# Kernel optimization log

Measured on AMD Instinct MI355X. Metric: run time of the kernel, lower is better.

## Reference

```python
import jax, jax.numpy as jnp
import numpy as np

N = 50000      # nodes
E = 800000     # edges (avg degree 16)
D_IN, D_H, D_OUT = 128, 256, 128


def setup_inputs() -> dict:
    key = jax.random.key(0)
    ks = jax.random.split(key, 8)
    x = jax.random.normal(ks[0], (N, D_IN), dtype=jnp.float32)
    edge_index = jax.random.randint(ks[1], (2, E), 0, N, dtype=jnp.int64)
    s1 = 1.0 / np.sqrt(D_IN).astype(np.float32)
    s2 = 1.0 / np.sqrt(D_H).astype(np.float32)
    return {
        "x": x,
        "edge_index": edge_index,
        "W1l": jax.random.normal(ks[2], (D_H, D_IN), jnp.float32) * s1,
        "b1l": jnp.zeros((D_H,), jnp.float32),
        "W1r": jax.random.normal(ks[3], (D_H, D_IN), jnp.float32) * s1,
        "W2l": jax.random.normal(ks[4], (D_OUT, D_H), jnp.float32) * s2,
        "b2l": jnp.zeros((D_OUT,), jnp.float32),
        "W2r": jax.random.normal(ks[5], (D_OUT, D_H), jnp.float32) * s2,
    }


def sage_conv(x, src, dst, Wl, bl, Wr):
    # mean-aggregate source features into destination nodes
    agg = jax.ops.segment_sum(x[src], dst, num_segments=N)           # [N, d_in]
    deg = jax.ops.segment_sum(jnp.ones((src.shape[0],), x.dtype), dst, num_segments=N)
    mean = agg / jnp.maximum(deg, 1.0)[:, None]
    # lin_l(mean_agg) + lin_r(x_root); lin_r has no bias (PyG SAGEConv default)
    return mean @ Wl.T + bl + x @ Wr.T


def reference(x, edge_index, W1l, b1l, W1r, W2l, b2l, W2r):
    src, dst = edge_index[0], edge_index[1]
    h = sage_conv(x, src, dst, W1l, b1l, W1r)
    h = jax.nn.relu(h)  # dropout inactive in eval mode
    return sage_conv(h, src, dst, W2l, b2l, W2r)
```

## Files before the change

kernel.cpp:

```cpp
#include <hip/hip_runtime.h>


typedef __attribute__((ext_vector_type(8))) short bf16x8;
typedef __attribute__((ext_vector_type(4))) float floatx4;

__device__ inline unsigned short f2b(float f) {
  unsigned int x = __float_as_uint(f);
  unsigned int r = (x + 0x7fffu + ((x >> 16) & 1u)) >> 16;
  return (unsigned short)r;
}
__device__ inline float blo(unsigned int u) { return __uint_as_float(u << 16); }
__device__ inline float bhi(unsigned int u) { return __uint_as_float(u & 0xffff0000u); }

#define ACC8(A, u)                                            \
  {                                                           \
    A[0] += blo((u).x); A[1] += bhi((u).x);                   \
    A[2] += blo((u).y); A[3] += bhi((u).y);                   \
    A[4] += blo((u).z); A[5] += bhi((u).z);                   \
    A[6] += blo((u).w); A[7] += bhi((u).w);                   \
  }

__global__ void prep_kernel(const float* __restrict__ x,
                            const float* __restrict__ W1l, const float* __restrict__ W1r,
                            const float* __restrict__ W2l, const float* __restrict__ W2r,
                            unsigned short* __restrict__ Wc1, unsigned short* __restrict__ Wc2,
                            unsigned short* __restrict__ A1,
                            int* __restrict__ cnt, int* __restrict__ off, int N, int E) {
  int i = blockIdx.x * blockDim.x + threadIdx.x;
  if (i < 65536) {
    int j = i >> 8, k = i & 255;
    float v1 = (k < 128) ? W1l[j * 128 + k] : W1r[j * 128 + (k - 128)];
    Wc1[i] = f2b(v1);
    float v2 = (j < 128) ? W2l[j * 256 + k] : W2r[(j - 128) * 256 + k];
    Wc2[i] = f2b(v2);
  }
  if (i < N) cnt[i] = 0;
  if (i == 0) off[N] = E;
  if (i < N * 32) {
    int n = i >> 5, c = (i & 31) * 4;
    float4 v = *(const float4*)(x + (size_t)n * 128 + c);
    uint2 p;
    p.x = (unsigned int)f2b(v.x) | ((unsigned int)f2b(v.y) << 16);
    p.y = (unsigned int)f2b(v.z) | ((unsigned int)f2b(v.w) << 16);
    *(uint2*)(A1 + (size_t)n * 256 + 128 + c) = p;
  }
}

__global__ void hist_kernel(const int* __restrict__ dst, int* __restrict__ cnt,
                            int* __restrict__ rank, int E) {
  int i = blockIdx.x * blockDim.x + threadIdx.x;
  int e = i * 4;
  if (e + 3 < E) {
    int4 d = *(const int4*)(dst + e);
    int4 r;
    r.x = atomicAdd(&cnt[d.x], 1);
    r.y = atomicAdd(&cnt[d.y], 1);
    r.z = atomicAdd(&cnt[d.z], 1);
    r.w = atomicAdd(&cnt[d.w], 1);
    *(int4*)(rank + e) = r;
  } else {
    for (; e < E; e++) rank[e] = atomicAdd(&cnt[dst[e]], 1);
  }
}

__global__ __launch_bounds__(1024) void scan_blocks_kernel(const int* __restrict__ cnt,
                                                           int* __restrict__ off,
                                                           int* __restrict__ bsum, int N) {
  __shared__ int wsum[16];
  __shared__ int wincl[16];
  const int tid = threadIdx.x;
  const int lane = tid & 63;
  const int wv = tid >> 6;
  const int i = blockIdx.x * 1024 + tid;
  const int v = (i < N) ? cnt[i] : 0;
  int s = v;
#pragma unroll
  for (int o = 1; o < 64; o <<= 1) {
    int t = __shfl_up(s, o, 64);
    if (lane >= o) s += t;
  }
  if (lane == 63) wsum[wv] = s;
  __syncthreads();
  if (tid < 16) {
    int ws = wsum[tid];
#pragma unroll
    for (int o = 1; o < 16; o <<= 1) {
      int t = __shfl_up(ws, o, 16);
      if ((tid & 15) >= o) ws += t;
    }
    wincl[tid] = ws;
  }
  __syncthreads();
  const int wo = wv ? wincl[wv - 1] : 0;
  if (i < N) off[i] = wo + s - v;
  if (tid == 1023) bsum[blockIdx.x] = wo + s;
}

__global__ __launch_bounds__(1024) void scan_add_kernel(int* __restrict__ off,
                                                        const int* __restrict__ bsum, int N, int SB) {
  __shared__ int bofs[64];
  const int tid = threadIdx.x;
  if (tid < 64) {
    int v = (tid < SB) ? bsum[tid] : 0;
    int s = v;
#pragma unroll
    for (int o = 1; o < 64; o <<= 1) {
      int t = __shfl_up(s, o, 64);
      if (tid >= o) s += t;
    }
    bofs[tid] = s - v;
  }
  __syncthreads();
  int i = blockIdx.x * 1024 + tid;
  if (i < N) off[i] = off[i] + bofs[blockIdx.x];
}

__global__ void fill_kernel(const int* __restrict__ src, const int* __restrict__ dst,
                            const int* __restrict__ rank, const int* __restrict__ off,
                            int* __restrict__ csr, int E) {
  int i = blockIdx.x * blockDim.x + threadIdx.x;
  int e = i * 4;
  if (e + 3 < E) {
    int4 d = *(const int4*)(dst + e);
    int4 r = *(const int4*)(rank + e);
    int4 s = *(const int4*)(src + e);
    csr[off[d.x] + r.x] = s.x;
    csr[off[d.y] + r.y] = s.y;
    csr[off[d.z] + r.z] = s.z;
    csr[off[d.w] + r.w] = s.w;
  } else {
    for (; e < E; e++) csr[off[dst[e]] + rank[e]] = src[e];
  }
}

__global__ void gather1_kernel(const unsigned short* __restrict__ feat,
                               const int* __restrict__ csr, const int* __restrict__ off,
                               unsigned short* __restrict__ ob, int N) {
  int wid = (blockIdx.x * blockDim.x + threadIdx.x) >> 6;
  if (wid >= N) return;
  const int lane = threadIdx.x & 63;
  const int slot = lane >> 3;
  const int j = lane & 7;
  const int c0 = j * 8;
  const int s0 = off[wid], s1 = off[wid + 1];
  float a[16] = {};
  int e = s0 + slot;
  for (; e + 8 < s1; e += 16) {
    int i0 = csr[e], i1 = csr[e + 8];
    uint4 u0 = *(const uint4*)(feat + (size_t)i0 * 256 + c0);
    uint4 v0 = *(const uint4*)(feat + (size_t)i0 * 256 + 64 + c0);
    uint4 u1 = *(const uint4*)(feat + (size_t)i1 * 256 + c0);
    uint4 v1 = *(const uint4*)(feat + (size_t)i1 * 256 + 64 + c0);
    ACC8(a, u0); ACC8((a + 8), v0);
    ACC8(a, u1); ACC8((a + 8), v1);
  }
  for (; e < s1; e += 8) {
    int i0 = csr[e];
    uint4 u0 = *(const uint4*)(feat + (size_t)i0 * 256 + c0);
    uint4 v0 = *(const uint4*)(feat + (size_t)i0 * 256 + 64 + c0);
    ACC8(a, u0); ACC8((a + 8), v0);
  }
#pragma unroll
  for (int k = 0; k < 16; k++) {
    a[k] += __shfl_xor(a[k], 8, 64);
    a[k] += __shfl_xor(a[k], 16, 64);
    a[k] += __shfl_xor(a[k], 32, 64);
  }
  if (slot == 0) {
    const float inv = 1.0f / fmaxf((float)(s1 - s0), 1.0f);
    uint4 p;
    p.x = (unsigned int)f2b(a[0] * inv) | ((unsigned int)f2b(a[1] * inv) << 16);
    p.y = (unsigned int)f2b(a[2] * inv) | ((unsigned int)f2b(a[3] * inv) << 16);
    p.z = (unsigned int)f2b(a[4] * inv) | ((unsigned int)f2b(a[5] * inv) << 16);
    p.w = (unsigned int)f2b(a[6] * inv) | ((unsigned int)f2b(a[7] * inv) << 16);
    *(uint4*)(ob + (size_t)wid * 256 + c0) = p;
    p.x = (unsigned int)f2b(a[8] * inv) | ((unsigned int)f2b(a[9] * inv) << 16);
    p.y = (unsigned int)f2b(a[10] * inv) | ((unsigned int)f2b(a[11] * inv) << 16);
    p.z = (unsigned int)f2b(a[12] * inv) | ((unsigned int)f2b(a[13] * inv) << 16);
    p.w = (unsigned int)f2b(a[14] * inv) | ((unsigned int)f2b(a[15] * inv) << 16);
    *(uint4*)(ob + (size_t)wid * 256 + 64 + c0) = p;
  }
}

__global__ void gather2_kernel(const unsigned short* __restrict__ t,
                               const int* __restrict__ csr, const int* __restrict__ off,
                               float* __restrict__ out, int N) {
  int wid = (blockIdx.x * blockDim.x + threadIdx.x) >> 6;
  if (wid >= N) return;
  const int lane = threadIdx.x & 63;
  const int slot = lane >> 3;
  const int j = lane & 7;
  const int c0 = j * 8;
  const int s0 = off[wid], s1 = off[wid + 1];
  float a[16] = {};
  int e = s0 + slot;
  for (; e + 8 < s1; e += 16) {
    int i0 = csr[e], i1 = csr[e + 8];
    uint4 u0 = *(const uint4*)(t + (size_t)i0 * 128 + c0);
    uint4 v0 = *(const uint4*)(t + (size_t)i0 * 128 + 64 + c0);
    uint4 u1 = *(const uint4*)(t + (size_t)i1 * 128 + c0);
    uint4 v1 = *(const uint4*)(t + (size_t)i1 * 128 + 64 + c0);
    ACC8(a, u0); ACC8((a + 8), v0);
    ACC8(a, u1); ACC8((a + 8), v1);
  }
  for (; e < s1; e += 8) {
    int i0 = csr[e];
    uint4 u0 = *(const uint4*)(t + (size_t)i0 * 128 + c0);
    uint4 v0 = *(const uint4*)(t + (size_t)i0 * 128 + 64 + c0);
    ACC8(a, u0); ACC8((a + 8), v0);
  }
#pragma unroll
  for (int k = 0; k < 16; k++) {
    a[k] += __shfl_xor(a[k], 8, 64);
    a[k] += __shfl_xor(a[k], 16, 64);
    a[k] += __shfl_xor(a[k], 32, 64);
  }
  if (slot == 0) {
    const float inv = 1.0f / fmaxf((float)(s1 - s0), 1.0f);
    float4* o0 = (float4*)(out + (size_t)wid * 128 + c0);
    float4* o1 = (float4*)(out + (size_t)wid * 128 + 64 + c0);
    float4 r0 = o0[0], r1 = o0[1], r2 = o1[0], r3 = o1[1];
    r0.x += a[0] * inv;  r0.y += a[1] * inv;  r0.z += a[2] * inv;  r0.w += a[3] * inv;
    r1.x += a[4] * inv;  r1.y += a[5] * inv;  r1.z += a[6] * inv;  r1.w += a[7] * inv;
    r2.x += a[8] * inv;  r2.y += a[9] * inv;  r2.z += a[10] * inv; r2.w += a[11] * inv;
    r3.x += a[12] * inv; r3.y += a[13] * inv; r3.z += a[14] * inv; r3.w += a[15] * inv;
    o0[0] = r0; o0[1] = r1; o1[0] = r2; o1[1] = r3;
  }
}

template <int MODE>
__global__ __launch_bounds__(256, 2)
void gemm_bf16(const unsigned short* __restrict__ A, const unsigned short* __restrict__ W,
               const float* __restrict__ bias, unsigned short* __restrict__ Hout,
               float* __restrict__ Fout, int M) {
  constexpr int LDA = 72;
  __shared__ __align__(16) unsigned short As[128 * LDA];
  __shared__ __align__(16) unsigned short Ws[128 * LDA];
  const int t = threadIdx.x;
  const int lane = t & 63;
  const int wave = t >> 6;
  const int wm = (wave & 1) * 64;
  const int wn = (wave >> 1) * 64;
  const int l15 = lane & 15;
  const int quad = lane >> 4;
  const int m_blk = blockIdx.x * 128;
  const int j_blk = blockIdx.y * 128;

  floatx4 acc[4][4] = {};

  for (int kc = 0; kc < 256; kc += 64) {
    __syncthreads();
#pragma unroll
    for (int i = 0; i < 4; i++) {
      int c = t + 256 * i;
      int row = c >> 3;
      int col = (c & 7) * 8;
      int ar = m_blk + row;
      if (ar >= M) ar = M - 1;
      uint4 av = *(const uint4*)(A + (size_t)ar * 256 + kc + col);
      *(uint4*)(As + row * LDA + col) = av;
      uint4 wv = *(const uint4*)(W + (size_t)(j_blk + row) * 256 + kc + col);
      *(uint4*)(Ws + row * LDA + col) = wv;
    }
    __syncthreads();
#pragma unroll
    for (int ks = 0; ks < 64; ks += 32) {
      bf16x8 af[4], bfr[4];
#pragma unroll
      for (int mt = 0; mt < 4; mt++)
        af[mt] = *(const bf16x8*)(As + (wm + mt * 16 + l15) * LDA + ks + quad * 8);
#pragma unroll
      for (int nt = 0; nt < 4; nt++)
        bfr[nt] = *(const bf16x8*)(Ws + (wn + nt * 16 + l15) * LDA + ks + quad * 8);
#pragma unroll
      for (int mt = 0; mt < 4; mt++)
#pragma unroll
        for (int nt = 0; nt < 4; nt++)
          acc[mt][nt] = __builtin_amdgcn_mfma_f32_16x16x32_bf16(af[mt], bfr[nt], acc[mt][nt], 0, 0, 0);
    }
  }

#pragma unroll
  for (int mt = 0; mt < 4; mt++) {
#pragma unroll
    for (int nt = 0; nt < 4; nt++) {
      const int jl = wn + nt * 16 + l15;
      float bv = 0.f;
      if (MODE == 0) bv = bias[j_blk + jl];
      else if (j_blk != 0) bv = bias[jl];
#pragma unroll
      for (int r = 0; r < 4; r++) {
        const int node = m_blk + wm + mt * 16 + quad * 4 + r;
        if (node >= M) continue;
        const float v = acc[mt][nt][r];
        if (MODE == 0) {
          Hout[(size_t)node * 256 + j_blk + jl] = f2b(fmaxf(v + bv, 0.f));
        } else if (j_blk == 0) {
          Hout[(size_t)node * 128 + jl] = f2b(v);
        } else {
          Fout[(size_t)node * 128 + jl] = v + bv;
        }
      }
    }
  }
}

extern "C" void kernel_launch(void* const* d_in, const int* in_sizes, int n_in,
                              void* d_out, int out_size, void* d_ws, size_t ws_size,
                              hipStream_t stream) {
  const float* x   = (const float*)d_in[0];
  const int*  eidx = (const int*)d_in[1];
  const float* W1l = (const float*)d_in[2];
  const float* b1l = (const float*)d_in[3];
  const float* W1r = (const float*)d_in[4];
  const float* W2l = (const float*)d_in[5];
  const float* b2l = (const float*)d_in[6];
  const float* W2r = (const float*)d_in[7];
  float* out = (float*)d_out;

  const int N = in_sizes[0] / 128;
  const int E = in_sizes[1] / 2;
  const int* src = eidx;
  const int* dst = eidx + E;

  int* cnt  = (int*)d_ws;
  int* off  = cnt + N;
  int* bsum = off + N + 1;
  int* rank = bsum + 64;
  int* csr  = rank + E;
  size_t ioff = ((size_t)(N + N + 1 + 64 + 2 * E) * 4 + 15) & ~(size_t)15;
  unsigned short* A1  = (unsigned short*)((char*)d_ws + ioff);
  unsigned short* h   = A1 + (size_t)N * 256;
  unsigned short* tb  = h + (size_t)N * 256;
  unsigned short* Wc1 = tb + (size_t)N * 128;
  unsigned short* Wc2 = Wc1 + 65536;

  const int SB = (N + 1023) / 1024;

  prep_kernel<<<(N * 32 + 255) / 256, 256, 0, stream>>>(x, W1l, W1r, W2l, W2r,
                                                        Wc1, Wc2, A1, cnt, off, N, E);
  hist_kernel<<<(E / 4 + 255) / 256, 256, 0, stream>>>(dst, cnt, rank, E);
  scan_blocks_kernel<<<SB, 1024, 0, stream>>>(cnt, off, bsum, N);
  scan_add_kernel<<<SB, 1024, 0, stream>>>(off, bsum, N, SB);
  fill_kernel<<<(E / 4 + 255) / 256, 256, 0, stream>>>(src, dst, rank, off, csr, E);

  const int gblocks = (N + 3) / 4;
  gather1_kernel<<<gblocks, 256, 0, stream>>>(A1 + 128, csr, off, A1, N);

  dim3 gg((N + 127) / 128, 2);
  gemm_bf16<0><<<gg, 256, 0, stream>>>(A1, Wc1, b1l, h, nullptr, N);
  gemm_bf16<1><<<gg, 256, 0, stream>>>(h, Wc2, b2l, tb, out, N);
  gather2_kernel<<<gblocks, 256, 0, stream>>>(tb, csr, off, out, N);
}
```

Baseline: 274.1 us.

## Fuse CSR build and first gather into one cooperative persistent kernel

Merges prep, histogram, two-level scan, CSR fill and the layer-1 gather into a single cooperative kernel that uses grid-wide syncs between phases instead of six separate launches. The scan is rewritten for 256-thread blocks handling 4 elements per thread, with the block offset taken as a prefix of the block sums. This targets per-launch overhead and the tail bubbles between short dependent kernels. In exchange it adds grid.sync costs and host-side occupancy queries on every call, and the grid-stride persistent loops may be less efficient than the original wide launches. It falls back to the old launch sequence if the cooperative launch fails.

Result: slower. 812.9 us (+196.6%).

```diff
diff --git a/kernel.cpp b/kernel.cpp
--- a/kernel.cpp
+++ b/kernel.cpp
@@ -1,4 +1,7 @@
 #include <hip/hip_runtime.h>
+#include <hip/hip_cooperative_groups.h>
+
+namespace cg = cooperative_groups;
 
 
 typedef __attribute__((ext_vector_type(8))) short bf16x8;
@@ -20,47 +23,221 @@
     A[6] += blo((u).w); A[7] += bhi((u).w);                   \
   }
 
+
+__device__ inline void ph_prep(int tid, int nthreads,
+                               const float* __restrict__ x,
+                               const float* __restrict__ W1l, const float* __restrict__ W1r,
+                               const float* __restrict__ W2l, const float* __restrict__ W2r,
+                               unsigned short* __restrict__ Wc1, unsigned short* __restrict__ Wc2,
+                               unsigned short* __restrict__ A1,
+                               int* __restrict__ cnt, int* __restrict__ off, int N, int E) {
+  for (int i = tid; i < N * 32; i += nthreads) {
+    int n = i >> 5, c = (i & 31) * 4;
+    float4 v = *(const float4*)(x + (size_t)n * 128 + c);
+    uint2 p;
+    p.x = (unsigned int)f2b(v.x) | ((unsigned int)f2b(v.y) << 16);
+    p.y = (unsigned int)f2b(v.z) | ((unsigned int)f2b(v.w) << 16);
+    *(uint2*)(A1 + (size_t)n * 256 + 128 + c) = p;
+  }
+  for (int i = tid; i < 65536; i += nthreads) {
+    int j = i >> 8, k = i & 255;
+    float v1 = (k < 128) ? W1l[j * 128 + k] : W1r[j * 128 + (k - 128)];
+    Wc1[i] = f2b(v1);
+    float v2 = (j < 128) ? W2l[j * 256 + k] : W2r[(j - 128) * 256 + k];
+    Wc2[i] = f2b(v2);
+  }
+  for (int i = tid; i < N; i += nthreads) cnt[i] = 0;
+  if (tid == 0) off[N] = E;
+}
+
+__device__ inline void ph_hist(int tid, int nthreads, const int* __restrict__ dst,
+                               int* __restrict__ cnt, int* __restrict__ rank, int E) {
+  for (int e = tid * 4; e < E; e += nthreads * 4) {
+    if (e + 3 < E) {
+      int4 d = *(const int4*)(dst + e);
+      int4 r;
+      r.x = atomicAdd(&cnt[d.x], 1);
+      r.y = atomicAdd(&cnt[d.y], 1);
+      r.z = atomicAdd(&cnt[d.z], 1);
+      r.w = atomicAdd(&cnt[d.w], 1);
+      *(int4*)(rank + e) = r;
+    } else {
+      for (int q = e; q < E; q++) rank[q] = atomicAdd(&cnt[dst[q]], 1);
+    }
+  }
+}
+
+__device__ inline void ph_fill(int tid, int nthreads,
+                               const int* __restrict__ src, const int* __restrict__ dst,
+                               const int* __restrict__ rank, const int* __restrict__ off,
+                               int* __restrict__ csr, int E) {
+  for (int e = tid * 4; e < E; e += nthreads * 4) {
+    if (e + 3 < E) {
+      int4 d = *(const int4*)(dst + e);
+      int4 r = *(const int4*)(rank + e);
+      int4 s4 = *(const int4*)(src + e);
+      csr[off[d.x] + r.x] = s4.x;
+      csr[off[d.y] + r.y] = s4.y;
+      csr[off[d.z] + r.z] = s4.z;
+      csr[off[d.w] + r.w] = s4.w;
+    } else {
+      for (int q = e; q < E; q++) csr[off[dst[q]] + rank[q]] = src[q];
+    }
+  }
+}
+
+__device__ inline void ph_gather1_one(int wid, int lane,
+                                      const unsigned short* __restrict__ feat,
+                                      const int* __restrict__ csr, const int* __restrict__ off,
+                                      unsigned short* __restrict__ A1) {
+  const int slot = lane >> 3;
+  const int c0 = (lane & 7) * 8;
+  const int s0 = off[wid], s1 = off[wid + 1];
+  float a[16] = {};
+  int e = s0 + slot;
+  for (; e + 8 < s1; e += 16) {
+    int i0 = csr[e], i1 = csr[e + 8];
+    uint4 u0 = *(const uint4*)(feat + (size_t)i0 * 256 + c0);
+    uint4 v0 = *(const uint4*)(feat + (size_t)i0 * 256 + 64 + c0);
+    uint4 u1 = *(const uint4*)(feat + (size_t)i1 * 256 + c0);
+    uint4 v1 = *(const uint4*)(feat + (size_t)i1 * 256 + 64 + c0);
+    ACC8(a, u0); ACC8((a + 8), v0);
+    ACC8(a, u1); ACC8((a + 8), v1);
+  }
+  for (; e < s1; e += 8) {
+    int i0 = csr[e];
+    uint4 u0 = *(const uint4*)(feat + (size_t)i0 * 256 + c0);
+    uint4 v0 = *(const uint4*)(feat + (size_t)i0 * 256 + 64 + c0);
+    ACC8(a, u0); ACC8((a + 8), v0);
+  }
+#pragma unroll
+  for (int k = 0; k < 16; k++) {
+    a[k] += __shfl_xor(a[k], 8, 64);
+    a[k] += __shfl_xor(a[k], 16, 64);
+    a[k] += __shfl_xor(a[k], 32, 64);
+  }
+  if (slot == 0) {
+    const float inv = 1.0f / fmaxf((float)(s1 - s0), 1.0f);
+    uint4 p;
+    p.x = (unsigned int)f2b(a[0] * inv) | ((unsigned int)f2b(a[1] * inv) << 16);
+    p.y = (unsigned int)f2b(a[2] * inv) | ((unsigned int)f2b(a[3] * inv) << 16);
+    p.z = (unsigned int)f2b(a[4] * inv) | ((unsigned int)f2b(a[5] * inv) << 16);
+    p.w = (unsigned int)f2b(a[6] * inv) | ((unsigned int)f2b(a[7] * inv) << 16);
+    *(uint4*)(A1 + (size_t)wid * 256 + c0) = p;
+    p.x = (unsigned int)f2b(a[8] * inv) | ((unsigned int)f2b(a[9] * inv) << 16);
+    p.y = (unsigned int)f2b(a[10] * inv) | ((unsigned int)f2b(a[11] * inv) << 16);
+    p.z = (unsigned int)f2b(a[12] * inv) | ((unsigned int)f2b(a[13] * inv) << 16);
+    p.w = (unsigned int)f2b(a[14] * inv) | ((unsigned int)f2b(a[15] * inv) << 16);
+    *(uint4*)(A1 + (size_t)wid * 256 + 64 + c0) = p;
+  }
+}
+
+__global__ __launch_bounds__(256, 8)
+void build_gather_kernel(const float* __restrict__ x,
+                         const float* __restrict__ W1l, const float* __restrict__ W1r,
+                         const float* __restrict__ W2l, const float* __restrict__ W2r,
+                         unsigned short* __restrict__ Wc1, unsigned short* __restrict__ Wc2,
+                         unsigned short* __restrict__ A1,
+                         int* __restrict__ cnt, int* __restrict__ off,
+                         int* __restrict__ bsum, int* __restrict__ rank,
+                         int* __restrict__ csr,
+                         const int* __restrict__ src, const int* __restrict__ dst,
+                         int N, int E, int SB) {
+  cg::grid_group grid = cg::this_grid();
+  __shared__ int wsum[4];
+  __shared__ int bofsS;
+  const int tid = blockIdx.x * blockDim.x + threadIdx.x;
+  const int nthreads = gridDim.x * blockDim.x;
+
+  ph_prep(tid, nthreads, x, W1l, W1r, W2l, W2r, Wc1, Wc2, A1, cnt, off, N, E);
+  grid.sync();
+  ph_hist(tid, nthreads, dst, cnt, rank, E);
+  grid.sync();
+
+  const int b = blockIdx.x;
+  if (b < SB) {
+    const int base = b * 1024 + threadIdx.x * 4;
+    int4 v = make_int4(0, 0, 0, 0);
+    if (base + 3 < N) v = *(const int4*)(cnt + base);
+    else {
+      if (base < N) v.x = cnt[base];
+      if (base + 1 < N) v.y = cnt[base + 1];
+      if (base + 2 < N) v.z = cnt[base + 2];
+    }
+    const int tsum = v.x + v.y + v.z + v.w;
+    const int lane = threadIdx.x & 63;
+    const int wv = threadIdx.x >> 6;
+    int s = tsum;
+#pragma unroll
+    for (int o = 1; o < 64; o <<= 1) {
+      int t = __shfl_up(s, o, 64);
+      if (lane >= o) s += t;
+    }
+    if (lane == 63) wsum[wv] = s;
+    __syncthreads();
+    int wo = 0;
+#pragma unroll
+    for (int w = 0; w < 4; w++) wo += (w < wv) ? wsum[w] : 0;
+    const int excl = wo + s - tsum;
+    int4 o4;
+    o4.x = excl; o4.y = excl + v.x; o4.z = o4.y + v.y; o4.w = o4.z + v.z;
+    if (base + 3 < N) *(int4*)(off + base) = o4;
+    else {
+      if (base < N) off[base] = o4.x;
+      if (base + 1 < N) off[base + 1] = o4.y;
+      if (base + 2 < N) off[base + 2] = o4.z;
+    }
+    if (threadIdx.x == 255) bsum[b] = wo + s;
+  }
+  grid.sync();
+
+  if (b > 0 && b < SB) {
+    if (threadIdx.x < 64) {
+      int v = (threadIdx.x < b) ? bsum[threadIdx.x] : 0;
+#pragma unroll
+      for (int o = 1; o < 64; o <<= 1) v += __shfl_xor(v, o, 64);
+      if (threadIdx.x == 0) bofsS = v;
+    }
+    __syncthreads();
+    const int bofs = bofsS;
+    const int base = b * 1024 + threadIdx.x * 4;
+    if (base + 3 < N) {
+      int4 o4 = *(const int4*)(off + base);
+      o4.x += bofs; o4.y += bofs; o4.z += bofs; o4.w += bofs;
+      *(int4*)(off + base) = o4;
+    } else {
+      if (base < N) off[base] += bofs;
+      if (base + 1 < N) off[base + 1] += bofs;
+      if (base + 2 < N) off[base + 2] += bofs;
+    }
+  }
+  grid.sync();
+
+  ph_fill(tid, nthreads, src, dst, rank, off, csr, E);
+  grid.sync();
+
+  const int nwaves = nthreads >> 6;
+  const int lane = threadIdx.x & 63;
+  const unsigned short* feat = A1 + 128;
+  for (int wid = tid >> 6; wid < N; wid += nwaves)
+    ph_gather1_one(wid, lane, feat, csr, off, A1);
+}
+
+
 __global__ void prep_kernel(const float* __restrict__ x,
                             const float* __restrict__ W1l, const float* __restrict__ W1r,
                             const float* __restrict__ W2l, const float* __restrict__ W2r,
                             unsigned short* __restrict__ Wc1, unsigned short* __restrict__ Wc2,
                             unsigned short* __restrict__ A1,
                             int* __restrict__ cnt, int* __restrict__ off, int N, int E) {
-  int i = blockIdx.x * blockDim.x + threadIdx.x;
-  if (i < 65536) {
-    int j = i >> 8, k = i & 255;
-    float v1 = (k < 128) ? W1l[j * 128 + k] : W1r[j * 128 + (k - 128)];
-    Wc1[i] = f2b(v1);
-    float v2 = (j < 128) ? W2l[j * 256 + k] : W2r[(j - 128) * 256 + k];
-    Wc2[i] = f2b(v2);
-  }
-  if (i < N) cnt[i] = 0;
-  if (i == 0) off[N] = E;
-  if (i < N * 32) {
-    int n = i >> 5, c = (i & 31) * 4;
-    float4 v = *(const float4*)(x + (size_t)n * 128 + c);
-    uint2 p;
-    p.x = (unsigned int)f2b(v.x) | ((unsigned int)f2b(v.y) << 16);
-    p.y = (unsigned int)f2b(v.z) | ((unsigned int)f2b(v.w) << 16);
-    *(uint2*)(A1 + (size_t)n * 256 + 128 + c) = p;
-  }
+  int tid = blockIdx.x * blockDim.x + threadIdx.x;
+  ph_prep(tid, gridDim.x * blockDim.x, x, W1l, W1r, W2l, W2r, Wc1, Wc2, A1, cnt, off, N, E);
 }
 
 __global__ void hist_kernel(const int* __restrict__ dst, int* __restrict__ cnt,
                             int* __restrict__ rank, int E) {
-  int i = blockIdx.x * blockDim.x + threadIdx.x;
-  int e = i * 4;
-  if (e + 3 < E) {
-    int4 d = *(const int4*)(dst + e);
-    int4 r;
-    r.x = atomicAdd(&cnt[d.x], 1);
-    r.y = atomicAdd(&cnt[d.y], 1);
-    r.z = atomicAdd(&cnt[d.z], 1);
-    r.w = atomicAdd(&cnt[d.w], 1);
-    *(int4*)(rank + e) = r;
-  } else {
-    for (; e < E; e++) rank[e] = atomicAdd(&cnt[dst[e]], 1);
-  }
+  int tid = blockIdx.x * blockDim.x + threadIdx.x;
+  ph_hist(tid, gridDim.x * blockDim.x, dst, cnt, rank, E);
 }
 
 __global__ __launch_bounds__(1024) void scan_blocks_kernel(const int* __restrict__ cnt,
@@ -118,68 +295,16 @@
 __global__ void fill_kernel(const int* __restrict__ src, const int* __restrict__ dst,
                             const int* __restrict__ rank, const int* __restrict__ off,
                             int* __restrict__ csr, int E) {
-  int i = blockIdx.x * blockDim.x + threadIdx.x;
-  int e = i * 4;
-  if (e + 3 < E) {
-    int4 d = *(const int4*)(dst + e);
-    int4 r = *(const int4*)(rank + e);
-    int4 s = *(const int4*)(src + e);
-    csr[off[d.x] + r.x] = s.x;
-    csr[off[d.y] + r.y] = s.y;
-    csr[off[d.z] + r.z] = s.z;
-    csr[off[d.w] + r.w] = s.w;
-  } else {
-    for (; e < E; e++) csr[off[dst[e]] + rank[e]] = src[e];
-  }
+  int tid = blockIdx.x * blockDim.x + threadIdx.x;
+  ph_fill(tid, gridDim.x * blockDim.x, src, dst, rank, off, csr, E);
 }
 
 __global__ void gather1_kernel(const unsigned short* __restrict__ feat,
                                const int* __restrict__ csr, const int* __restrict__ off,
-                               unsigned short* __restrict__ ob, int N) {
+                               unsigned short* __restrict__ A1, int N) {
   int wid = (blockIdx.x * blockDim.x + threadIdx.x) >> 6;
   if (wid >= N) return;
-  const int lane = threadIdx.x & 63;
-  const int slot = lane >> 3;
-  const int j = lane & 7;
-  const int c0 = j * 8;
-  const int s0 = off[wid], s1 = off[wid + 1];
-  float a[16] = {};
-  int e = s0 + slot;
-  for (; e + 8 < s1; e += 16) {
-    int i0 = csr[e], i1 = csr[e + 8];
-    uint4 u0 = *(const uint4*)(feat + (size_t)i0 * 256 + c0);
-    uint4 v0 = *(const uint4*)(feat + (size_t)i0 * 256 + 64 + c0);
-    uint4 u1 = *(const uint4*)(feat + (size_t)i1 * 256 + c0);
-    uint4 v1 = *(const uint4*)(feat + (size_t)i1 * 256 + 64 + c0);
-    ACC8(a, u0); ACC8((a + 8), v0);
-    ACC8(a, u1); ACC8((a + 8), v1);
-  }
-  for (; e < s1; e += 8) {
-    int i0 = csr[e];
-    uint4 u0 = *(const uint4*)(feat + (size_t)i0 * 256 + c0);
-    uint4 v0 = *(const uint4*)(feat + (size_t)i0 * 256 + 64 + c0);
-    ACC8(a, u0); ACC8((a + 8), v0);
-  }
-#pragma unroll
-  for (int k = 0; k < 16; k++) {
-    a[k] += __shfl_xor(a[k], 8, 64);
-    a[k] += __shfl_xor(a[k], 16, 64);
-    a[k] += __shfl_xor(a[k], 32, 64);
-  }
-  if (slot == 0) {
-    const float inv = 1.0f / fmaxf((float)(s1 - s0), 1.0f);
-    uint4 p;
-    p.x = (unsigned int)f2b(a[0] * inv) | ((unsigned int)f2b(a[1] * inv) << 16);
-    p.y = (unsigned int)f2b(a[2] * inv) | ((unsigned int)f2b(a[3] * inv) << 16);
-    p.z = (unsigned int)f2b(a[4] * inv) | ((unsigned int)f2b(a[5] * inv) << 16);
-    p.w = (unsigned int)f2b(a[6] * inv) | ((unsigned int)f2b(a[7] * inv) << 16);
-    *(uint4*)(ob + (size_t)wid * 256 + c0) = p;
-    p.x = (unsigned int)f2b(a[8] * inv) | ((unsigned int)f2b(a[9] * inv) << 16);
-    p.y = (unsigned int)f2b(a[10] * inv) | ((unsigned int)f2b(a[11] * inv) << 16);
-    p.z = (unsigned int)f2b(a[12] * inv) | ((unsigned int)f2b(a[13] * inv) << 16);
-    p.w = (unsigned int)f2b(a[14] * inv) | ((unsigned int)f2b(a[15] * inv) << 16);
-    *(uint4*)(ob + (size_t)wid * 256 + 64 + c0) = p;
-  }
+  ph_gather1_one(wid, threadIdx.x & 63, feat, csr, off, A1);
 }
 
 __global__ void gather2_kernel(const unsigned short* __restrict__ t,
@@ -189,8 +314,7 @@
   if (wid >= N) return;
   const int lane = threadIdx.x & 63;
   const int slot = lane >> 3;
-  const int j = lane & 7;
-  const int c0 = j * 8;
+  const int c0 = (lane & 7) * 8;
   const int s0 = off[wid], s1 = off[wid + 1];
   float a[16] = {};
   int e = s0 + slot;
@@ -318,8 +442,8 @@
   const float* W2r = (const float*)d_in[7];
   float* out = (float*)d_out;
 
-  const int N = in_sizes[0] / 128;
-  const int E = in_sizes[1] / 2;
+  int N = in_sizes[0] / 128;
+  int E = in_sizes[1] / 2;
   const int* src = eidx;
   const int* dst = eidx + E;
 
@@ -335,20 +459,44 @@
   unsigned short* Wc1 = tb + (size_t)N * 128;
   unsigned short* Wc2 = Wc1 + 65536;
 
-  const int SB = (N + 1023) / 1024;
-
-  prep_kernel<<<(N * 32 + 255) / 256, 256, 0, stream>>>(x, W1l, W1r, W2l, W2r,
-                                                        Wc1, Wc2, A1, cnt, off, N, E);
-  hist_kernel<<<(E / 4 + 255) / 256, 256, 0, stream>>>(dst, cnt, rank, E);
-  scan_blocks_kernel<<<SB, 1024, 0, stream>>>(cnt, off, bsum, N);
-  scan_add_kernel<<<SB, 1024, 0, stream>>>(off, bsum, N, SB);
-  fill_kernel<<<(E / 4 + 255) / 256, 256, 0, stream>>>(src, dst, rank, off, csr, E);
-
-  const int gblocks = (N + 3) / 4;
-  gather1_kernel<<<gblocks, 256, 0, stream>>>(A1 + 128, csr, off, A1, N);
+  int SB = (N + 1023) / 1024;
+
+  int dev = 0;
+  (void)hipGetDevice(&dev);
+  int numCU = 0;
+  (void)hipDeviceGetAttribute(&numCU, hipDeviceAttributeMultiprocessorCount, dev);
+  int maxBlk = 0;
+  (void)hipOccupancyMaxActiveBlocksPerMultiprocessor(
+      &maxBlk, (const void*)build_gather_kernel, 256, 0);
+  long gridB = (long)maxBlk * (numCU > 0 ? numCU : 0);
+  if (gridB > 2048) gridB = 2048;
+
+  bool coop_ok = false;
+  if (gridB >= SB + 1) {
+    void* cargs[] = {(void*)&x, (void*)&W1l, (void*)&W1r, (void*)&W2l, (void*)&W2r,
+                     (void*)&Wc1, (void*)&Wc2, (void*)&A1,
+                     (void*)&cnt, (void*)&off, (void*)&bsum, (void*)&rank, (void*)&csr,
+                     (void*)&src, (void*)&dst, (void*)&N, (void*)&E, (void*)&SB};
+    hipError_t err = hipLaunchCooperativeKernel((const void*)build_gather_kernel,
+                                                dim3((unsigned)gridB), dim3(256),
+                                                cargs, 0, stream);
+    coop_ok = (err == hipSuccess);
+  }
+
+  if (!coop_ok) {
+    prep_kernel<<<(N * 32 + 255) / 256, 256, 0, stream>>>(x, W1l, W1r, W2l, W2r,
+                                                          Wc1, Wc2, A1, cnt, off, N, E);
+    hist_kernel<<<(E / 4 + 255) / 256, 256, 0, stream>>>(dst, cnt, rank, E);
+    scan_blocks_kernel<<<SB, 1024, 0, stream>>>(cnt, off, bsum, N);
+    scan_add_kernel<<<SB, 1024, 0, stream>>>(off, bsum, N, SB);
+    fill_kernel<<<(E / 4 + 255) / 256, 256, 0, stream>>>(src, dst, rank, off, csr, E);
+    gather1_kernel<<<(N + 3) / 4, 256, 0, stream>>>(A1 + 128, csr, off, A1, N);
+  }
 
   dim3 gg((N + 127) / 128, 2);
   gemm_bf16<0><<<gg, 256, 0, stream>>>(A1, Wc1, b1l, h, nullptr, N);
   gemm_bf16<1><<<gg, 256, 0, stream>>>(h, Wc2, b2l, tb, out, N);
+
+  const int gblocks = (N + 3) / 4;
   gather2_kernel<<<gblocks, 256, 0, stream>>>(tb, csr, off, out, N);
 }
```
